# Performance work log

Measured on AMD Instinct MI355X. Metric: run time of the kernel, lower is better.

The kernel has to match this reference:

```python
import jax, jax.numpy as jnp
import numpy as np

EPS = 1e-12  # F.normalize default eps


def _l2_normalize(x):
    # F.normalize(x, p=2) normalizes over dim=1 (channels) by default
    n = jnp.sqrt(jnp.sum(x * x, axis=1, keepdims=True))
    return x / jnp.maximum(n, EPS)


def _cost_volume(left, right, num_disp):
    # left, right: (N, C, H, W)
    l = _l2_normalize(left)
    r = _l2_normalize(right)
    # dot[n,h,x,y] = sum_c l[n,c,h,x] * r[n,c,h,y]   -> (N, H, W, W)
    dot = jnp.einsum('nchx,nchy->nhxy', l, r)
    W = left.shape[-1]
    x = jnp.arange(W)                                   # (W,)
    j = jnp.arange(num_disp)                            # (D,)
    # torch.diagonal(offset=-j) + F.pad((j,0)) picks dot[..., x, x-j] with zeros for x<j
    idx = jnp.clip(x[None, :] - j[:, None], 0, W - 1)   # (D, W)
    g = dot[:, :, x[None, :], idx]                      # (N, H, D, W)
    valid = (x[None, :] >= j[:, None])                  # (D, W)
    g = jnp.where(valid[None, None, :, :], g, jnp.zeros((), dtype=g.dtype))
    return jnp.transpose(g, (0, 2, 1, 3))               # (N, D, H, W)


def setup_inputs() -> dict:
    key = jax.random.key(0)
    ks = jax.random.split(key, 6)
    shapes = [(2, 32, 256, 512), (2, 64, 128, 256), (2, 96, 64, 128)]
    inp = {}
    for i, s in enumerate(shapes):
        inp[f'left{i}'] = jax.random.normal(ks[2 * i], s, dtype=jnp.float32)
        inp[f'right{i}'] = jax.random.normal(ks[2 * i + 1], s, dtype=jnp.float32)
    inp['max_disparity'] = 128
    return inp


def reference(left0, right0, left1, right1, left2, right2, max_disparity):
    lefts = [left0, left1, left2]
    rights = [right0, right1, right2]
    md = min(int(max_disparity), lefts[0].shape[-1])
    cost_volumes = []
    for i, (l, r) in enumerate(zip(lefts, rights)):
        cost_volumes.append(_cost_volume(l, r, md // (2 ** i)))
    return tuple(cost_volumes)
```

## Files before the change

### kernel.cpp

```cpp
#include <hip/hip_runtime.h>

#define EPSN 1e-12f

template<int C, int H, int W, int D, int TX, int NT>
__global__ __launch_bounds__(NT)
void cost_volume_kernel(const float* __restrict__ Lp, const float* __restrict__ Rp,
                        float* __restrict__ out)
{
    static_assert(TX == 64, "tile decode hardcodes TX=64");
    constexpr int RS = TX + D;
    constexpr int NTILES = (TX / 4) * (D / 4);

    __shared__ __align__(16) float ls[C * TX];
    __shared__ __align__(16) float rs[C * RS];

    const int tid = threadIdx.x;
    const int bx  = blockIdx.x;
    constexpr int NXB = W / TX;
    const int xb  = bx % NXB;
    const int h   = (bx / NXB) % H;
    const int n   = bx / (NXB * H);
    const int X0  = xb * TX;
    const int Yb  = X0 - D;

    {
        constexpr int NV = C * TX / 4;
        for (int i = tid; i < NV; i += NT) {
            const int c = i / (TX / 4);
            const int v = i % (TX / 4);
            const float4 val =
                *(const float4*)&Lp[(((size_t)n * C + c) * H + h) * W + X0 + 4 * v];
            *(float4*)&ls[c * TX + 4 * v] = val;
        }
    }
    {
        constexpr int NV = C * RS / 4;
        for (int i = tid; i < NV; i += NT) {
            const int c = i / (RS / 4);
            const int v = i % (RS / 4);
            const int y = Yb + 4 * v;
            const float* src = &Rp[(((size_t)n * C + c) * H + h) * W];
            float4 val;
            if (y >= 0) {
                val = *(const float4*)&src[y];
            } else {
                val.x = (y + 0) >= 0 ? src[y + 0] : 0.f;
                val.y = (y + 1) >= 0 ? src[y + 1] : 0.f;
                val.z = (y + 2) >= 0 ? src[y + 2] : 0.f;
                val.w = (y + 3) >= 0 ? src[y + 3] : 0.f;
            }
            *(float4*)&rs[c * RS + 4 * v] = val;
        }
    }
    __syncthreads();

    for (int col = tid; col < TX + RS; col += NT) {
        float* base;
        int stride;
        if (col < TX) { base = &ls[col];       stride = TX; }
        else          { base = &rs[col - TX];  stride = RS; }
        float s = 0.f;
        #pragma unroll 8
        for (int c = 0; c < C; ++c) { const float v = base[c * stride]; s += v * v; }
        const float inv = 1.0f / fmaxf(sqrtf(s), EPSN);
        #pragma unroll 8
        for (int c = 0; c < C; ++c) base[c * stride] *= inv;
    }
    __syncthreads();

    for (int t = tid; t < NTILES; t += NT) {
        const int gx = t & 15;
        const int tj = t >> 4;
        const int rbase = D + 4 * (gx - tj) - 4;

        float acc[4][4];
        #pragma unroll
        for (int a = 0; a < 4; ++a)
            #pragma unroll
            for (int b = 0; b < 4; ++b) acc[a][b] = 0.f;

        #pragma unroll 4
        for (int c = 0; c < C; ++c) {
            const float4 lv = *(const float4*)&ls[c * TX + 4 * gx];
            const float4 r0 = *(const float4*)&rs[c * RS + rbase];
            const float4 r1 = *(const float4*)&rs[c * RS + rbase + 4];
            const float lf[4] = {lv.x, lv.y, lv.z, lv.w};
            const float rf[8] = {r0.x, r0.y, r0.z, r0.w, r1.x, r1.y, r1.z, r1.w};
            #pragma unroll
            for (int jp = 0; jp < 4; ++jp)
                #pragma unroll
                for (int dx = 0; dx < 4; ++dx)
                    acc[jp][dx] = fmaf(lf[dx], rf[4 + dx - jp], acc[jp][dx]);
        }

        const int j0 = 4 * tj;
        float* orow = &out[(((size_t)n * D + j0) * H + h) * W + X0 + 4 * gx];
        #pragma unroll
        for (int jp = 0; jp < 4; ++jp) {
            const float4 v = {acc[jp][0], acc[jp][1], acc[jp][2], acc[jp][3]};
            *(float4*)&orow[(size_t)jp * H * W] = v;
        }
    }
}

extern "C" void kernel_launch(void* const* d_in, const int* in_sizes, int n_in,
                              void* d_out, int out_size, void* d_ws, size_t ws_size,
                              hipStream_t stream) {
    (void)in_sizes; (void)n_in; (void)d_ws; (void)ws_size; (void)out_size;
    const float* l0 = (const float*)d_in[0];
    const float* r0 = (const float*)d_in[1];
    const float* l1 = (const float*)d_in[2];
    const float* r1 = (const float*)d_in[3];
    const float* l2 = (const float*)d_in[4];
    const float* r2 = (const float*)d_in[5];

    float* o0 = (float*)d_out;
    float* o1 = o0 + (size_t)2 * 128 * 256 * 512;
    float* o2 = o1 + (size_t)2 * 64 * 128 * 256;

    cost_volume_kernel<32, 256, 512, 128, 64, 256>
        <<<2 * 256 * (512 / 64), 256, 0, stream>>>(l0, r0, o0);
    cost_volume_kernel<64, 128, 256, 64, 64, 256>
        <<<2 * 128 * (256 / 64), 256, 0, stream>>>(l1, r1, o1);
    cost_volume_kernel<96, 64, 128, 32, 64, 256>
        <<<2 * 64 * (128 / 64), 256, 0, stream>>>(l2, r2, o2);
}
```

Before: 316.4 us.

## Compute cost volume with bf16 MFMA tiles and LDS-staged coalesced output

Replaces the scalar FP32 FMA dot-product loop with 16x16x32 bf16 MFMA instructions. During normalization the features are converted to bf16 in a transposed shared-memory layout. Each wave computes 16x16 blocks of the x-by-y dot matrix along the band, scatters the diagonal entries into a shared output buffer, then writes that buffer out with coalesced float4 stores. The smaller levels now use 32-wide tiles and 128-thread blocks. The cost is bf16 precision loss on the correlation values and wasted MFMA work on the off-band parts of each tile.

```diff
diff --git a/kernel.cpp b/kernel.cpp
--- a/kernel.cpp
+++ b/kernel.cpp
@@ -1,105 +1,119 @@
 #include <hip/hip_runtime.h>
 
-#define EPSN 1e-12f
+typedef __attribute__((ext_vector_type(8))) short bf16x8;
+typedef __attribute__((ext_vector_type(4))) float f32x4;
+
+static __device__ __forceinline__ unsigned short f32_to_bf16(float f) {
+    unsigned int x = __float_as_uint(f);
+    x += 0x7fffu + ((x >> 16) & 1u);
+    return (unsigned short)(x >> 16);
+}
 
 template<int C, int H, int W, int D, int TX, int NT>
 __global__ __launch_bounds__(NT)
-void cost_volume_kernel(const float* __restrict__ Lp, const float* __restrict__ Rp,
-                        float* __restrict__ out)
+void cost_volume_mfma(const float* __restrict__ Lp, const float* __restrict__ Rp,
+                      float* __restrict__ out)
 {
-    static_assert(TX == 64, "tile decode hardcodes TX=64");
     constexpr int RS = TX + D;
-    constexpr int NTILES = (TX / 4) * (D / 4);
+    constexpr int AS = C + 8;
+    constexpr int KC = C / 32;
+    constexpr int NW = NT / 64;
+    static_assert(NW == TX / 16, "one wave per 16-wide x-tile");
+    static_assert((AS * 2) % 16 == 0, "frag rows must be 16B aligned");
 
-    __shared__ __align__(16) float ls[C * TX];
-    __shared__ __align__(16) float rs[C * RS];
+    constexpr int STAGE_F = C * (TX + RS);
+    constexpr int OBUF_F  = D * TX;
+    constexpr int UNION_F = STAGE_F > OBUF_F ? STAGE_F : OBUF_F;
+
+    __shared__ __align__(16) float uni[UNION_F];
+    __shared__ __align__(16) unsigned short Abf[RS * AS];
+    __shared__ __align__(16) unsigned short Bbf[TX * AS];
+
+    float* lsf  = uni;
+    float* rsf  = uni + C * TX;
+    float* obuf = uni;
 
     const int tid = threadIdx.x;
-    const int bx  = blockIdx.x;
     constexpr int NXB = W / TX;
-    const int xb  = bx % NXB;
-    const int h   = (bx / NXB) % H;
-    const int n   = bx / (NXB * H);
-    const int X0  = xb * TX;
-    const int Yb  = X0 - D;
+    const int bx = blockIdx.x;
+    const int xb = bx % NXB;
+    const int h  = (bx / NXB) % H;
+    const int n  = bx / (NXB * H);
+    const int X0 = xb * TX;
 
-    {
-        constexpr int NV = C * TX / 4;
-        for (int i = tid; i < NV; i += NT) {
-            const int c = i / (TX / 4);
-            const int v = i % (TX / 4);
-            const float4 val =
-                *(const float4*)&Lp[(((size_t)n * C + c) * H + h) * W + X0 + 4 * v];
-            *(float4*)&ls[c * TX + 4 * v] = val;
+    for (int i = tid; i < C * TX / 4; i += NT) {
+        const int c = i / (TX / 4), v = i % (TX / 4);
+        *(float4*)&lsf[c * TX + 4 * v] =
+            *(const float4*)&Lp[(((size_t)n * C + c) * H + h) * W + X0 + 4 * v];
+    }
+    for (int i = tid; i < C * RS / 4; i += NT) {
+        const int c = i / (RS / 4), v = i % (RS / 4);
+        const int y = X0 - D + 4 * v;
+        const float* src = &Rp[(((size_t)n * C + c) * H + h) * W];
+        float4 val;
+        if (y >= 0) val = *(const float4*)&src[y];
+        else {
+            val.x = (y + 0) >= 0 ? src[y + 0] : 0.f;
+            val.y = (y + 1) >= 0 ? src[y + 1] : 0.f;
+            val.z = (y + 2) >= 0 ? src[y + 2] : 0.f;
+            val.w = (y + 3) >= 0 ? src[y + 3] : 0.f;
         }
+        *(float4*)&rsf[c * RS + 4 * v] = val;
     }
-    {
-        constexpr int NV = C * RS / 4;
-        for (int i = tid; i < NV; i += NT) {
-            const int c = i / (RS / 4);
-            const int v = i % (RS / 4);
-            const int y = Yb + 4 * v;
-            const float* src = &Rp[(((size_t)n * C + c) * H + h) * W];
-            float4 val;
-            if (y >= 0) {
-                val = *(const float4*)&src[y];
-            } else {
-                val.x = (y + 0) >= 0 ? src[y + 0] : 0.f;
-                val.y = (y + 1) >= 0 ? src[y + 1] : 0.f;
-                val.z = (y + 2) >= 0 ? src[y + 2] : 0.f;
-                val.w = (y + 3) >= 0 ? src[y + 3] : 0.f;
-            }
-            *(float4*)&rs[c * RS + 4 * v] = val;
+    __syncthreads();
+
+    for (int col = tid; col < TX + RS; col += NT) {
+        const float* src; int stride; unsigned short* dst;
+        if (col < TX) { src = lsf + col;        stride = TX; dst = Bbf + col * AS; }
+        else          { src = rsf + (col - TX); stride = RS; dst = Abf + (col - TX) * AS; }
+        float v[C];
+        float s = 0.f;
+        #pragma unroll
+        for (int c = 0; c < C; ++c) { v[c] = src[c * stride]; s += v[c] * v[c]; }
+        const float inv = 1.0f / fmaxf(sqrtf(s), 1e-12f);
+        #pragma unroll
+        for (int c0 = 0; c0 < C; c0 += 8) {
+            union { unsigned short us[8]; uint4 q; } p;
+            #pragma unroll
+            for (int k = 0; k < 8; ++k) p.us[k] = f32_to_bf16(v[c0 + k] * inv);
+            *(uint4*)&dst[c0] = p.q;
         }
     }
     __syncthreads();
 
-    for (int col = tid; col < TX + RS; col += NT) {
-        float* base;
-        int stride;
-        if (col < TX) { base = &ls[col];       stride = TX; }
-        else          { base = &rs[col - TX];  stride = RS; }
-        float s = 0.f;
-        #pragma unroll 8
-        for (int c = 0; c < C; ++c) { const float v = base[c * stride]; s += v * v; }
-        const float inv = 1.0f / fmaxf(sqrtf(s), EPSN);
-        #pragma unroll 8
-        for (int c = 0; c < C; ++c) base[c * stride] *= inv;
+    const int wave = tid >> 6, lane = tid & 63;
+    const int colc = lane & 15, quad = lane >> 4;
+
+    bf16x8 bfr[KC];
+    #pragma unroll
+    for (int kc = 0; kc < KC; ++kc)
+        bfr[kc] = *(const bf16x8*)&Bbf[(wave * 16 + colc) * AS + kc * 32 + quad * 8];
+
+    const int xl = wave * 16 + colc;
+    #pragma unroll
+    for (int t = 0; t <= D / 16; ++t) {
+        const int yt = wave + t;
+        f32x4 acc = {0.f, 0.f, 0.f, 0.f};
+        #pragma unroll
+        for (int kc = 0; kc < KC; ++kc) {
+            const bf16x8 a =
+                *(const bf16x8*)&Abf[(yt * 16 + colc) * AS + kc * 32 + quad * 8];
+            acc = __builtin_amdgcn_mfma_f32_16x16x32_bf16(a, bfr[kc], acc, 0, 0, 0);
+        }
+        const int jb = D + xl - yt * 16 - quad * 4;
+        #pragma unroll
+        for (int r = 0; r < 4; ++r) {
+            const int j = jb - r;
+            if (j >= 0 && j < D) obuf[j * TX + xl] = acc[r];
+        }
     }
     __syncthreads();
 
-    for (int t = tid; t < NTILES; t += NT) {
-        const int gx = t & 15;
-        const int tj = t >> 4;
-        const int rbase = D + 4 * (gx - tj) - 4;
-
-        float acc[4][4];
-        #pragma unroll
-        for (int a = 0; a < 4; ++a)
-            #pragma unroll
-            for (int b = 0; b < 4; ++b) acc[a][b] = 0.f;
-
-        #pragma unroll 4
-        for (int c = 0; c < C; ++c) {
-            const float4 lv = *(const float4*)&ls[c * TX + 4 * gx];
-            const float4 r0 = *(const float4*)&rs[c * RS + rbase];
-            const float4 r1 = *(const float4*)&rs[c * RS + rbase + 4];
-            const float lf[4] = {lv.x, lv.y, lv.z, lv.w};
-            const float rf[8] = {r0.x, r0.y, r0.z, r0.w, r1.x, r1.y, r1.z, r1.w};
-            #pragma unroll
-            for (int jp = 0; jp < 4; ++jp)
-                #pragma unroll
-                for (int dx = 0; dx < 4; ++dx)
-                    acc[jp][dx] = fmaf(lf[dx], rf[4 + dx - jp], acc[jp][dx]);
-        }
-
-        const int j0 = 4 * tj;
-        float* orow = &out[(((size_t)n * D + j0) * H + h) * W + X0 + 4 * gx];
-        #pragma unroll
-        for (int jp = 0; jp < 4; ++jp) {
-            const float4 v = {acc[jp][0], acc[jp][1], acc[jp][2], acc[jp][3]};
-            *(float4*)&orow[(size_t)jp * H * W] = v;
-        }
+    constexpr int JV = TX / 4;
+    for (int i = tid; i < D * TX / 4; i += NT) {
+        const int j = i / JV, c4 = i % JV;
+        *(float4*)&out[(((size_t)n * D + j) * H + h) * W + X0 + 4 * c4] =
+            *(const float4*)&obuf[j * TX + 4 * c4];
     }
 }
 
@@ -118,10 +132,10 @@
     float* o1 = o0 + (size_t)2 * 128 * 256 * 512;
     float* o2 = o1 + (size_t)2 * 64 * 128 * 256;
 
-    cost_volume_kernel<32, 256, 512, 128, 64, 256>
+    cost_volume_mfma<32, 256, 512, 128, 64, 256>
         <<<2 * 256 * (512 / 64), 256, 0, stream>>>(l0, r0, o0);
-    cost_volume_kernel<64, 128, 256, 64, 64, 256>
-        <<<2 * 128 * (256 / 64), 256, 0, stream>>>(l1, r1, o1);
-    cost_volume_kernel<96, 64, 128, 32, 64, 256>
-        <<<2 * 64 * (128 / 64), 256, 0, stream>>>(l2, r2, o2);
+    cost_volume_mfma<64, 128, 256, 64, 32, 128>
+        <<<2 * 128 * (256 / 32), 128, 0, stream>>>(l1, r1, o1);
+    cost_volume_mfma<96, 64, 128, 32, 32, 128>
+        <<<2 * 64 * (128 / 32), 128, 0, stream>>>(l2, r2, o2);
 }
```

Result: no change. 312.2 us (-1.3%).
